# Kernel optimization log

Measured on AMD Instinct MI355X. Metric: run time of the kernel, lower is better.

Reference implementation:

```python
import jax, jax.numpy as jnp
import numpy as np

N = 1048576        # number of raw proposals
NC = 2             # num classes (source hardcodes self.nc = 2)
CONF_THRES = 0.25  # score_thres
IOU_THRES = 0.45
MAX_WH = 4096.0    # class offset for class-aware NMS (agnostic=False)
MAX_NMS = 30000    # cap on boxes entering NMS
MAX_DET = 300      # cap on detections returned


def setup_inputs() -> dict:
    key = jax.random.key(0)
    k1, k2, k3, k4 = jax.random.split(key, 4)
    xy = jax.random.uniform(k1, (1, N, 2), dtype=jnp.float32) * 640.0          # box centers (pixels)
    wh = jax.random.uniform(k2, (1, N, 2), dtype=jnp.float32) * 98.0 + 2.0     # widths/heights in [2, 100]
    obj = jax.random.uniform(k3, (1, N, 1), dtype=jnp.float32)                 # objectness
    cls = jax.random.uniform(k4, (1, N, NC), dtype=jnp.float32)                # class scores
    prediction = jnp.concatenate([xy, wh, obj, cls], axis=-1)                  # [1, N, 4+1+nc]
    return {"prediction": prediction}


def reference(prediction):
    # Single image (source only ever fills/returns output[0]).
    pred = prediction[0]                        # [N, 7]
    obj = pred[:, 4]                            # objectness
    cls = pred[:, 5:5 + NC] * obj[:, None]      # conf = obj * cls  (nc > 1 branch)
    conf = jnp.max(cls, axis=-1)                # best-class confidence
    j = jnp.argmax(cls, axis=-1)                # best-class index

    # xywh -> xyxy
    xy, wh = pred[:, :2], pred[:, 2:4]
    box = jnp.concatenate([xy - wh * 0.5, xy + wh * 0.5], axis=-1)  # [N, 4]

    # candidate mask: obj > thres (xc) AND best-class conf > thres
    valid = (obj > CONF_THRES) & (conf > CONF_THRES)
    scores = jnp.where(valid, conf, -1.0)

    # n > max_nms: keep top MAX_NMS by confidence (argsort descending truncation)
    top_s, top_i = jax.lax.top_k(scores, MAX_NMS)       # [MAX_NMS]
    box_t = box[top_i]                                   # [MAX_NMS, 4]
    conf_t = conf[top_i]
    j_t = j[top_i]

    # class-aware NMS: offset boxes per class so classes never suppress each other
    boxes_off = box_t + (j_t.astype(box_t.dtype) * MAX_WH)[:, None]
    area = (boxes_off[:, 2] - boxes_off[:, 0]) * (boxes_off[:, 3] - boxes_off[:, 1])

    # Greedy NMS: iteratively select max-score box, suppress IoU > thres.
    # Selecting the argmax each step is equivalent to sorted greedy NMS, and
    # MAX_DET steps yields exactly the first max_det kept indices.
    def step(s, _):
        idx = jnp.argmax(s)
        ok = s[idx] > 0.0                       # any real candidate left?
        b = boxes_off[idx]
        lt = jnp.maximum(b[:2], boxes_off[:, :2])
        rb = jnp.minimum(b[2:], boxes_off[:, 2:])
        inter = jnp.prod(jnp.clip(rb - lt, 0.0), axis=-1)
        iou = inter / (area[idx] + area - inter)
        s = jnp.where(ok & (iou > IOU_THRES), -1.0, s)  # suppress (incl. self, IoU=1)
        return s, (idx, ok)

    _, (sel, ok) = jax.lax.scan(step, top_s, None, length=MAX_DET)

    dets = jnp.concatenate(
        [box_t[sel], conf_t[sel, None], j_t[sel, None].astype(box_t.dtype)], axis=-1
    )                                           # [MAX_DET, 6] = [xyxy, conf, cls]
    dets = dets * ok[:, None].astype(dets.dtype)  # zero out padding rows
    return dets, ok
```

## Files before the change

kernel.cpp:

```cpp
#include <hip/hip_runtime.h>
#include <stdint.h>

#pragma clang fp contract(off)

#define N_ELEM   1048576
#define MAX_NMS  30000
#define MAX_DET  300
#define IOU_T    0.45f
#define CONF_T   0.25f
#define SOA_N    30720
#define KMIN     0xBE800000u
#define EQCAP    2048
#define RPW      16

typedef uint32_t u32;
typedef unsigned long long u64;

#define C_CB   0
#define C_KP   1
#define C_A    2
#define C_NUM  3
#define C_EQC  4

__device__ inline u32 monokey(float s){
  u32 b = __float_as_uint(s);
  return b ^ ((b & 0x80000000u) ? 0xFFFFFFFFu : 0x80000000u);
}
__device__ inline int binOf(u32 k){
  u32 d = (k - KMIN) >> 8;
  return d > 65535u ? 65535 : (int)d;
}
__device__ inline u64 shfl64(u64 v, int src){
  int lo = __shfl((int)(u32)(v & 0xFFFFFFFFull), src);
  int hi = __shfl((int)(u32)(v >> 32), src);
  return ((u64)(u32)hi << 32) | (u32)lo;
}

__global__ void kkeys(const float4* __restrict__ pred4, u32* __restrict__ keys,
                      u32* __restrict__ hist){
  __shared__ float lds[1792];
  int t = threadIdx.x;
  const float4* src = pred4 + (size_t)blockIdx.x * 448;
  float4* l4 = (float4*)lds;
  #pragma unroll
  for (int k = 0; k < 2; k++){
    int idx = k*256 + t;
    if (idx < 448) l4[idx] = src[idx];
  }
  __syncthreads();
  float obj = lds[t*7 + 4], c0 = lds[t*7 + 5], c1 = lds[t*7 + 6];
  float p0 = c0*obj, p1 = c1*obj;
  float conf = fmaxf(p0, p1);
  bool valid = (obj > CONF_T) && (conf > CONF_T);
  float score = valid ? conf : -1.0f;
  u32 mk = monokey(score);
  keys[blockIdx.x*256 + t] = mk;
  if (mk > KMIN) atomicAdd(&hist[binOf(mk)], 1u);
}

__global__ void kchunks(const u32* __restrict__ hist, u32* __restrict__ chunkSum){
  int gw = (blockIdx.x*blockDim.x + threadIdx.x) >> 6;
  int lane = threadIdx.x & 63;
  if (gw >= 1024) return;
  u32 v = hist[gw*64 + lane];
  #pragma unroll
  for (int off = 32; off > 0; off >>= 1) v += __shfl_down(v, off);
  if (lane == 0) chunkSum[gw] = v;
}

__global__ void kpick(const u32* __restrict__ chunkSum, const u32* __restrict__ hist,
                      u32* __restrict__ chunkAbove, u32* __restrict__ ctrl){
  __shared__ u32 s[1024];
  __shared__ int selC;
  __shared__ u32 selAbove;
  __shared__ u32 chunk[64];
  int t = threadIdx.x;
  u32 own = chunkSum[t];
  s[t] = own; __syncthreads();
  for (int off = 1; off < 1024; off <<= 1){
    u32 v = s[t];
    u32 add = (t + off < 1024) ? s[t + off] : 0u;
    __syncthreads();
    s[t] = v + add;
    __syncthreads();
  }
  u32 above = s[t] - own;
  chunkAbove[t] = above;
  u32 grand = s[0];
  const u32 K = MAX_NMS;
  if (grand >= K){
    if (above < K && K <= above + own){ selC = t; selAbove = above; }
  }
  __syncthreads();
  if (grand >= K && t < 64) chunk[t] = hist[selC*64 + t];
  __syncthreads();
  if (t == 0){
    if (grand < K){
      ctrl[C_CB] = 0xFFFFFFFFu; ctrl[C_KP] = 0; ctrl[C_A] = grand; ctrl[C_NUM] = grand;
    } else {
      u32 cum = selAbove;
      for (int b = 63; b >= 0; b--){
        u32 c = chunk[b];
        if (cum + c >= K){
          ctrl[C_CB] = (u32)(selC*64 + b);
          ctrl[C_KP] = K - cum;
          ctrl[C_A]  = cum;
          ctrl[C_NUM] = K;
          break;
        }
        cum += c;
      }
    }
  }
}

__global__ void kbinbase(const u32* __restrict__ hist, const u32* __restrict__ chunkAbove,
                         u32* __restrict__ binBase){
  int gw = (blockIdx.x*blockDim.x + threadIdx.x) >> 6;
  int lane = threadIdx.x & 63;
  if (gw >= 1024) return;
  u32 v = hist[gw*64 + lane];
  u32 suf = v;
  #pragma unroll
  for (int off = 1; off < 64; off <<= 1){
    u32 o = __shfl_down(suf, off);
    suf += (lane + off < 64) ? o : 0u;
  }
  binBase[gw*64 + lane] = chunkAbove[gw] + suf - v;
}

__global__ void kscatter(const uint4* __restrict__ keys4, const u32* __restrict__ binBase,
                         u32* __restrict__ binCursor, u32* __restrict__ ctrl,
                         u32* __restrict__ binnedKey, u32* __restrict__ binnedIdx,
                         u32* __restrict__ eqKey, u32* __restrict__ eqIdx){
  int t = blockIdx.x*blockDim.x + threadIdx.x;
  if (t >= N_ELEM/4) return;
  int cb = (int)ctrl[C_CB];
  uint4 kv = keys4[t];
  u32 kk[4] = {kv.x, kv.y, kv.z, kv.w};
  #pragma unroll
  for (int r = 0; r < 4; r++){
    u32 k = kk[r];
    if (k <= KMIN) continue;
    int b = binOf(k);
    u32 i = (u32)(t*4 + r);
    if (b > cb){
      u32 pos = binBase[b] + atomicAdd(&binCursor[b], 1u);
      if (pos < MAX_NMS){ binnedKey[pos] = k; binnedIdx[pos] = i; }
    } else if (b == cb){
      u32 e = atomicAdd(&ctrl[C_EQC], 1u);
      if (e < EQCAP){ eqKey[e] = k; eqIdx[e] = i; }
    }
  }
}

__global__ void keq(u32* __restrict__ ctrl, const u32* __restrict__ eqKey,
                    const u32* __restrict__ eqIdx, u32* __restrict__ binnedKey,
                    u32* __restrict__ binnedIdx, u32* __restrict__ binHist){
  u32 Kp = ctrl[C_KP];
  if (Kp == 0) return;
  u32 cb = ctrl[C_CB], A = ctrl[C_A];
  u32 n = ctrl[C_EQC]; if (n > EQCAP) n = EQCAP;
  int lane = threadIdx.x;
  for (u32 e = (u32)lane; e < n; e += 64){
    u32 k = eqKey[e], i = eqIdx[e];
    u32 r = 0;
    for (u32 m = 0; m < n; m++){
      u32 km = eqKey[m], im = eqIdx[m];
      r += (km > k) || (km == k && im < i);
    }
    if (r < Kp){ binnedKey[A + r] = k; binnedIdx[A + r] = i; }
  }
  if (lane == 0) binHist[cb] = Kp;
}

__global__ void krank(const float* __restrict__ pred, const u32* __restrict__ binnedKey,
                      const u32* __restrict__ binnedIdx, const u32* __restrict__ binBase,
                      const u32* __restrict__ binHist, const u32* __restrict__ ctrl,
                      float* __restrict__ soa){
  int p = blockIdx.x*blockDim.x + threadIdx.x;
  int numCand = (int)ctrl[C_NUM];
  if (p >= numCand) return;
  u32 k = binnedKey[p]; u32 i = binnedIdx[p];
  if (i >= N_ELEM) i = 0;
  int b = binOf(k);
  u32 st = binBase[b], cnt = binHist[b];
  u32 r = st;
  for (u32 q = st; q < st + cnt; q++){
    u32 kq = binnedKey[q], iq = binnedIdx[q];
    if (kq > k || (kq == k && iq < i)) r++;
  }
  if (r >= (u32)numCand) return;
  const float* row = pred + (size_t)i*7;
  float x = row[0], y = row[1], w = row[2], hh = row[3];
  float obj = row[4], c0 = row[5], c1 = row[6];
  float p0 = c0*obj, p1 = c1*obj;
  float conf = fmaxf(p0, p1);
  float jf = (p0 >= p1) ? 0.0f : 1.0f;
  float bx1 = x - w*0.5f, by1 = y - hh*0.5f;
  float bx2 = x + w*0.5f, by2 = y + hh*0.5f;
  float off = jf * 4096.0f;
  float ox1 = bx1 + off, oy1 = by1 + off, ox2 = bx2 + off, oy2 = by2 + off;
  float area = (ox2 - ox1) * (oy2 - oy1);
  soa[r + 0*SOA_N] = ox1;  soa[r + 1*SOA_N] = oy1;
  soa[r + 2*SOA_N] = ox2;  soa[r + 3*SOA_N] = oy2;
  soa[r + 4*SOA_N] = area; soa[r + 5*SOA_N] = conf;
  soa[r + 6*SOA_N] = jf;
  soa[r + 7*SOA_N] = bx1;  soa[r + 8*SOA_N] = by1;
  soa[r + 9*SOA_N] = bx2;  soa[r +10*SOA_N] = by2;
}

__global__ void kmask(const float* __restrict__ soa, u64* __restrict__ mask,
                      int W, int WBsh, int nUnits){
  int lane = threadIdx.x & 63;
  int gw = (blockIdx.x*blockDim.x + threadIdx.x) >> 6;
  int nwaves = (gridDim.x*blockDim.x) >> 6;
  int WB = 1 << WBsh;
  for (int u = gw; u < nUnits; u += nwaves){
    int rowg = u >> WBsh;
    int w = u & (WB - 1);
    if (((w + 1) << 6) <= rowg*RPW) continue;
    int j = (w << 6) + lane;
    float cx1 = soa[j], cy1 = soa[j + SOA_N], cx2 = soa[j + 2*SOA_N],
          cy2 = soa[j + 3*SOA_N], ca = soa[j + 4*SOA_N];
    #pragma unroll
    for (int rr = 0; rr < RPW; rr++){
      int i = rowg*RPW + rr;
      if (w < (i >> 6)) continue;
      float rx1 = soa[i], ry1 = soa[i + SOA_N], rx2 = soa[i + 2*SOA_N],
            ry2 = soa[i + 3*SOA_N], ra = soa[i + 4*SOA_N];
      float ltx = fmaxf(rx1, cx1), lty = fmaxf(ry1, cy1);
      float rbx = fminf(rx2, cx2), rby = fminf(ry2, cy2);
      float iw = fmaxf(rbx - ltx, 0.0f), ih = fmaxf(rby - lty, 0.0f);
      float inter = iw * ih;
      float iou = inter / ((ra + ca) - inter);
      u64 m = __ballot(iou > IOU_T);
      if (lane == 0) mask[(size_t)i*WB + w] = m;
    }
  }
}

__global__ void __launch_bounds__(64) kwalk(const float* __restrict__ soa,
                                            const u64* __restrict__ mask,
                                            const u32* __restrict__ ctrl,
                                            float* __restrict__ out, int out_size,
                                            int W){
  __shared__ float kx1[320], ky1[320], kx2[320], ky2[320], ka[320];
  __shared__ u64 dlds[64];
  int lane = threadIdx.x;
  for (int o = lane; o < out_size; o += 64) out[o] = 0.0f;
  int numCand = (int)ctrl[C_NUM];
  int WB = W >> 6;
  int lim = numCand < W ? numCand : W;
  int nb = (lim + 63) >> 6;
  u64 rem0 = 0, rem1 = 0;
  int nsel = 0;

  u64 diag = 0;
  if (nb > 0 && lane < lim) diag = mask[(size_t)lane*WB + 0];

  for (int bi = 0; bi < nb && nsel < MAX_DET; bi++){
    u64 remw = (bi < 64) ? shfl64(rem0, bi) : shfl64(rem1, bi - 64);
    u64 w = ~remw;
    int rb = lim - (bi << 6);
    if (rb < 64) w &= ((1ull << rb) - 1ull);
    dlds[lane] = diag;
    __syncthreads();

    u64 diagn = 0;
    int inext = (bi + 1)*64 + lane;
    if (bi + 1 < nb && inext < lim) diagn = mask[(size_t)inext*WB + (bi + 1)];

    u64 sel = 0;
    int room = MAX_DET - nsel;
    while (w){
      int b = (int)__builtin_ctzll(w);
      sel |= (1ull << b);
      if (--room == 0) break;
      u64 rw = dlds[b];
      w &= ~rw;
      w &= ~(1ull << b);
    }
    int cnt = __popcll(sel);

    u64 s = sel;
    long long ids[8];
    #pragma unroll
    for (int q = 0; q < 8; q++){
      if (s){ ids[q] = (long long)((bi << 6) + __builtin_ctzll(s)); s &= s - 1; }
      else ids[q] = -1;
    }
    u64 a0[8], a1[8];
    #pragma unroll
    for (int q = 0; q < 8; q++){
      a0[q] = 0; a1[q] = 0;
      if (ids[q] >= 0){
        const u64* rp = mask + (size_t)ids[q]*WB;
        if (lane < WB)      a0[q] = rp[lane];
        if (64 + lane < WB) a1[q] = rp[64 + lane];
      }
    }

    if (lane < cnt){
      u64 t = sel;
      for (int q = 0; q < lane; q++) t &= t - 1;
      int b = (int)__builtin_ctzll(t);
      int i = (bi << 6) + b;
      int r = nsel + lane;
      kx1[r] = soa[i];            ky1[r] = soa[i + SOA_N];
      kx2[r] = soa[i + 2*SOA_N];  ky2[r] = soa[i + 3*SOA_N];
      ka[r]  = soa[i + 4*SOA_N];
      float* dr = out + r*6;
      dr[0] = soa[i + 7*SOA_N];  dr[1] = soa[i + 8*SOA_N];
      dr[2] = soa[i + 9*SOA_N];  dr[3] = soa[i + 10*SOA_N];
      dr[4] = soa[i + 5*SOA_N];  dr[5] = soa[i + 6*SOA_N];
      out[MAX_DET*6 + r] = 1.0f;
    }
    nsel += cnt;

    #pragma unroll
    for (int q = 0; q < 8; q++){ rem0 |= a0[q]; rem1 |= a1[q]; }

    while (s){
      long long ids2[8];
      #pragma unroll
      for (int q = 0; q < 8; q++){
        if (s){ ids2[q] = (long long)((bi << 6) + __builtin_ctzll(s)); s &= s - 1; }
        else ids2[q] = -1;
      }
      u64 b0[8], b1[8];
      #pragma unroll
      for (int q = 0; q < 8; q++){
        b0[q] = 0; b1[q] = 0;
        if (ids2[q] >= 0){
          const u64* rp = mask + (size_t)ids2[q]*WB;
          if (lane < WB)      b0[q] = rp[lane];
          if (64 + lane < WB) b1[q] = rp[64 + lane];
        }
      }
      #pragma unroll
      for (int q = 0; q < 8; q++){ rem0 |= b0[q]; rem1 |= b1[q]; }
    }
    diag = diagn;
    __syncthreads();
  }

  if (nsel < MAX_DET && numCand > W){
    for (int base = W; base < numCand && nsel < MAX_DET; base += 64){
      int li = base + lane;
      bool has = li < numCand;
      float cox1=0.f,coy1=0.f,cox2=0.f,coy2=0.f,car=1.f,csc=-1.f,ccl=0.f;
      float cbx1=0.f,cby1=0.f,cbx2=0.f,cby2=0.f;
      if (has){
        cox1 = soa[li]; coy1 = soa[li + SOA_N]; cox2 = soa[li + 2*SOA_N];
        coy2 = soa[li + 3*SOA_N]; car = soa[li + 4*SOA_N];
        csc = soa[li + 5*SOA_N]; ccl = soa[li + 6*SOA_N];
        cbx1 = soa[li + 7*SOA_N]; cby1 = soa[li + 8*SOA_N];
        cbx2 = soa[li + 9*SOA_N]; cby2 = soa[li + 10*SOA_N];
      }
      int m = min(64, numCand - base);
      for (int t2 = 0; t2 < m && nsel < MAX_DET; t2++){
        float qx1 = __shfl(cox1, t2), qy1 = __shfl(coy1, t2);
        float qx2 = __shfl(cox2, t2), qy2 = __shfl(coy2, t2);
        float qa  = __shfl(car,  t2);
        bool supp = false;
        #pragma unroll
        for (int q = 0; q < 5; q++){
          int slot = lane + (q << 6);
          if (slot < nsel){
            float ltx = fmaxf(qx1, kx1[slot]), lty = fmaxf(qy1, ky1[slot]);
            float rbx = fminf(qx2, kx2[slot]), rby = fminf(qy2, ky2[slot]);
            float iw = fmaxf(rbx - ltx, 0.0f), ih = fmaxf(rby - lty, 0.0f);
            float inter = iw * ih;
            float iou = inter / ((qa + ka[slot]) - inter);
            supp = supp || (iou > IOU_T);
          }
        }
        if (__any(supp)) continue;
        float bx1 = __shfl(cbx1, t2), by1 = __shfl(cby1, t2);
        float bx2 = __shfl(cbx2, t2), by2 = __shfl(cby2, t2);
        float sc  = __shfl(csc,  t2), cl  = __shfl(ccl,  t2);
        if (lane == 0){
          kx1[nsel] = qx1; ky1[nsel] = qy1; kx2[nsel] = qx2; ky2[nsel] = qy2; ka[nsel] = qa;
          float* dr = out + nsel*6;
          dr[0] = bx1; dr[1] = by1; dr[2] = bx2; dr[3] = by2; dr[4] = sc; dr[5] = cl;
          out[MAX_DET*6 + nsel] = 1.0f;
        }
        nsel++;
      }
    }
  }
}

extern "C" void kernel_launch(void* const* d_in, const int* in_sizes, int n_in,
                              void* d_out, int out_size, void* d_ws, size_t ws_size,
                              hipStream_t stream){
  const float* pred = (const float*)d_in[0];
  float* out = (float*)d_out;
  char* w = (char*)d_ws;

  u32*  keys       = (u32*)(w + 0x000000);
  u32*  hist       = (u32*)(w + 0x400000);
  u32*  binCursor  = (u32*)(w + 0x440000);
  u32*  ctrl       = (u32*)(w + 0x480000);
  u32*  chunkSum   = (u32*)(w + 0x484000);
  u32*  chunkAbove = (u32*)(w + 0x488000);
  u32*  binBase    = (u32*)(w + 0x4C0000);
  u32*  eqKey      = (u32*)(w + 0x500000);
  u32*  eqIdx      = (u32*)(w + 0x502000);
  u32*  binnedKey  = (u32*)(w + 0x510000);
  u32*  binnedIdx  = (u32*)(w + 0x530000);
  float* soa       = (float*)(w + 0x550000);
  u64*  mask       = (u64*)(w + 0x6A0000);

  int W, WBsh;
  if      (ws_size >= 0xEA0000){ W = 8192; WBsh = 7; }
  else if (ws_size >= 0x8A0000){ W = 4096; WBsh = 6; }
  else                         { W = 2048; WBsh = 5; }

  hipMemsetAsync(hist, 0, 0x80100, stream);

  kkeys   <<<4096, 256, 0, stream>>>((const float4*)pred, keys, hist);
  kchunks <<<256, 256, 0, stream>>>(hist, chunkSum);
  kpick   <<<1, 1024, 0, stream>>>(chunkSum, hist, chunkAbove, ctrl);
  kbinbase<<<256, 256, 0, stream>>>(hist, chunkAbove, binBase);
  kscatter<<<1024, 256, 0, stream>>>((const uint4*)keys, binBase, binCursor, ctrl,
                                     binnedKey, binnedIdx, eqKey, eqIdx);
  keq     <<<1, 64, 0, stream>>>(ctrl, eqKey, eqIdx, binnedKey, binnedIdx, hist);
  krank   <<<(MAX_NMS + 255)/256, 256, 0, stream>>>(pred, binnedKey, binnedIdx, binBase,
                                                    hist, ctrl, soa);
  int nUnits = (W/RPW) << WBsh;
  kmask   <<<2048, 256, 0, stream>>>(soa, mask, W, WBsh, nUnits);
  kwalk   <<<1, 64, 0, stream>>>(soa, mask, ctrl, out, out_size, W);
}
```

Before: 285.9 us.

## Fuse chunk-sum, pick and bin-base kernels; fold tie-bin ranking into krank

Merges the three small histogram-scan kernels (kchunks, kpick, kbinbase) into one 1024-thread kselect kernel, so chunk sums and prefix offsets stay in shared memory. The single-wave keq kernel that ranked boundary-bin ties is removed; krank now ranks those ties in parallel across threads and writes their SoA rows directly. This cuts three kernel launches and their global round trips, and turns a serial 64-lane loop into a wide parallel pass. The cost is that the whole 64K-bin histogram is now read and scanned by a single workgroup, which may be slower than spreading it over 256 blocks.

Result: slower. 325.3 us (+13.8%).

```diff
diff --git a/kernel.cpp b/kernel.cpp
--- a/kernel.cpp
+++ b/kernel.cpp
@@ -58,24 +58,23 @@
   if (mk > KMIN) atomicAdd(&hist[binOf(mk)], 1u);
 }
 
-__global__ void kchunks(const u32* __restrict__ hist, u32* __restrict__ chunkSum){
-  int gw = (blockIdx.x*blockDim.x + threadIdx.x) >> 6;
-  int lane = threadIdx.x & 63;
-  if (gw >= 1024) return;
-  u32 v = hist[gw*64 + lane];
-  #pragma unroll
-  for (int off = 32; off > 0; off >>= 1) v += __shfl_down(v, off);
-  if (lane == 0) chunkSum[gw] = v;
-}
-
-__global__ void kpick(const u32* __restrict__ chunkSum, const u32* __restrict__ hist,
-                      u32* __restrict__ chunkAbove, u32* __restrict__ ctrl){
+__global__ void __launch_bounds__(1024) kselect(const u32* __restrict__ hist,
+                                                u32* __restrict__ binBase,
+                                                u32* __restrict__ ctrl){
+  __shared__ u32 csum[1024];
   __shared__ u32 s[1024];
   __shared__ int selC;
-  __shared__ u32 selAbove;
   __shared__ u32 chunk[64];
-  int t = threadIdx.x;
-  u32 own = chunkSum[t];
+  int t = threadIdx.x, lane = t & 63, wv = t >> 6;
+  for (int j = 0; j < 64; j++){
+    int c = wv*64 + j;
+    u32 v = hist[c*64 + lane];
+    #pragma unroll
+    for (int off = 32; off > 0; off >>= 1) v += __shfl_down(v, off);
+    if (lane == 0) csum[c] = v;
+  }
+  __syncthreads();
+  u32 own = csum[t];
   s[t] = own; __syncthreads();
   for (int off = 1; off < 1024; off <<= 1){
     u32 v = s[t];
@@ -85,12 +84,10 @@
     __syncthreads();
   }
   u32 above = s[t] - own;
-  chunkAbove[t] = above;
   u32 grand = s[0];
+  csum[t] = above;
   const u32 K = MAX_NMS;
-  if (grand >= K){
-    if (above < K && K <= above + own){ selC = t; selAbove = above; }
-  }
+  if (grand >= K && above < K && K <= above + own){ selC = t; }
   __syncthreads();
   if (grand >= K && t < 64) chunk[t] = hist[selC*64 + t];
   __syncthreads();
@@ -98,7 +95,7 @@
     if (grand < K){
       ctrl[C_CB] = 0xFFFFFFFFu; ctrl[C_KP] = 0; ctrl[C_A] = grand; ctrl[C_NUM] = grand;
     } else {
-      u32 cum = selAbove;
+      u32 cum = csum[selC];
       for (int b = 63; b >= 0; b--){
         u32 c = chunk[b];
         if (cum + c >= K){
@@ -112,21 +109,17 @@
       }
     }
   }
-}
-
-__global__ void kbinbase(const u32* __restrict__ hist, const u32* __restrict__ chunkAbove,
-                         u32* __restrict__ binBase){
-  int gw = (blockIdx.x*blockDim.x + threadIdx.x) >> 6;
-  int lane = threadIdx.x & 63;
-  if (gw >= 1024) return;
-  u32 v = hist[gw*64 + lane];
-  u32 suf = v;
-  #pragma unroll
-  for (int off = 1; off < 64; off <<= 1){
-    u32 o = __shfl_down(suf, off);
-    suf += (lane + off < 64) ? o : 0u;
-  }
-  binBase[gw*64 + lane] = chunkAbove[gw] + suf - v;
+  for (int j = 0; j < 64; j++){
+    int c = wv*64 + j;
+    u32 v = hist[c*64 + lane];
+    u32 suf = v;
+    #pragma unroll
+    for (int off = 1; off < 64; off <<= 1){
+      u32 o = __shfl_down(suf, off);
+      suf += (lane + off < 64) ? o : 0u;
+    }
+    binBase[c*64 + lane] = csum[c] + suf - v;
+  }
 }
 
 __global__ void kscatter(const uint4* __restrict__ keys4, const u32* __restrict__ binBase,
@@ -154,43 +147,8 @@
   }
 }
 
-__global__ void keq(u32* __restrict__ ctrl, const u32* __restrict__ eqKey,
-                    const u32* __restrict__ eqIdx, u32* __restrict__ binnedKey,
-                    u32* __restrict__ binnedIdx, u32* __restrict__ binHist){
-  u32 Kp = ctrl[C_KP];
-  if (Kp == 0) return;
-  u32 cb = ctrl[C_CB], A = ctrl[C_A];
-  u32 n = ctrl[C_EQC]; if (n > EQCAP) n = EQCAP;
-  int lane = threadIdx.x;
-  for (u32 e = (u32)lane; e < n; e += 64){
-    u32 k = eqKey[e], i = eqIdx[e];
-    u32 r = 0;
-    for (u32 m = 0; m < n; m++){
-      u32 km = eqKey[m], im = eqIdx[m];
-      r += (km > k) || (km == k && im < i);
-    }
-    if (r < Kp){ binnedKey[A + r] = k; binnedIdx[A + r] = i; }
-  }
-  if (lane == 0) binHist[cb] = Kp;
-}
-
-__global__ void krank(const float* __restrict__ pred, const u32* __restrict__ binnedKey,
-                      const u32* __restrict__ binnedIdx, const u32* __restrict__ binBase,
-                      const u32* __restrict__ binHist, const u32* __restrict__ ctrl,
-                      float* __restrict__ soa){
-  int p = blockIdx.x*blockDim.x + threadIdx.x;
-  int numCand = (int)ctrl[C_NUM];
-  if (p >= numCand) return;
-  u32 k = binnedKey[p]; u32 i = binnedIdx[p];
-  if (i >= N_ELEM) i = 0;
-  int b = binOf(k);
-  u32 st = binBase[b], cnt = binHist[b];
-  u32 r = st;
-  for (u32 q = st; q < st + cnt; q++){
-    u32 kq = binnedKey[q], iq = binnedIdx[q];
-    if (kq > k || (kq == k && iq < i)) r++;
-  }
-  if (r >= (u32)numCand) return;
+__device__ inline void writeSoA(const float* __restrict__ pred, float* __restrict__ soa,
+                                u32 r, u32 i){
   const float* row = pred + (size_t)i*7;
   float x = row[0], y = row[1], w = row[2], hh = row[3];
   float obj = row[4], c0 = row[5], c1 = row[6];
@@ -208,6 +166,39 @@
   soa[r + 6*SOA_N] = jf;
   soa[r + 7*SOA_N] = bx1;  soa[r + 8*SOA_N] = by1;
   soa[r + 9*SOA_N] = bx2;  soa[r +10*SOA_N] = by2;
+}
+
+__global__ void krank(const float* __restrict__ pred, const u32* __restrict__ binnedKey,
+                      const u32* __restrict__ binnedIdx, const u32* __restrict__ binBase,
+                      const u32* __restrict__ binHist, const u32* __restrict__ ctrl,
+                      const u32* __restrict__ eqKey, const u32* __restrict__ eqIdx,
+                      float* __restrict__ soa){
+  int p = blockIdx.x*blockDim.x + threadIdx.x;
+  u32 A = ctrl[C_A], Kp = ctrl[C_KP];
+  if (Kp > 0){
+    u32 n = ctrl[C_EQC]; if (n > EQCAP) n = EQCAP;
+    if (p < (int)n){
+      u32 k = eqKey[p], i = eqIdx[p];
+      u32 r = 0;
+      for (u32 m = 0; m < n; m++){
+        u32 km = eqKey[m], im = eqIdx[m];
+        r += (km > k) || (km == k && im < i);
+      }
+      if (r < Kp) writeSoA(pred, soa, A + r, i);
+    }
+  }
+  if (p < (int)A){
+    u32 k = binnedKey[p]; u32 i = binnedIdx[p];
+    if (i >= N_ELEM) i = 0;
+    int b = binOf(k);
+    u32 st = binBase[b], cnt = binHist[b];
+    u32 r = st;
+    for (u32 q = st; q < st + cnt; q++){
+      u32 kq = binnedKey[q], iq = binnedIdx[q];
+      if (kq > k || (kq == k && iq < i)) r++;
+    }
+    if (r < A) writeSoA(pred, soa, r, i);
+  }
 }
 
 __global__ void kmask(const float* __restrict__ soa, u64* __restrict__ mask,
@@ -403,8 +394,6 @@
   u32*  hist       = (u32*)(w + 0x400000);
   u32*  binCursor  = (u32*)(w + 0x440000);
   u32*  ctrl       = (u32*)(w + 0x480000);
-  u32*  chunkSum   = (u32*)(w + 0x484000);
-  u32*  chunkAbove = (u32*)(w + 0x488000);
   u32*  binBase    = (u32*)(w + 0x4C0000);
   u32*  eqKey      = (u32*)(w + 0x500000);
   u32*  eqIdx      = (u32*)(w + 0x502000);
@@ -421,14 +410,11 @@
   hipMemsetAsync(hist, 0, 0x80100, stream);
 
   kkeys   <<<4096, 256, 0, stream>>>((const float4*)pred, keys, hist);
-  kchunks <<<256, 256, 0, stream>>>(hist, chunkSum);
-  kpick   <<<1, 1024, 0, stream>>>(chunkSum, hist, chunkAbove, ctrl);
-  kbinbase<<<256, 256, 0, stream>>>(hist, chunkAbove, binBase);
+  kselect <<<1, 1024, 0, stream>>>(hist, binBase, ctrl);
   kscatter<<<1024, 256, 0, stream>>>((const uint4*)keys, binBase, binCursor, ctrl,
                                      binnedKey, binnedIdx, eqKey, eqIdx);
-  keq     <<<1, 64, 0, stream>>>(ctrl, eqKey, eqIdx, binnedKey, binnedIdx, hist);
-  krank   <<<(MAX_NMS + 255)/256, 256, 0, stream>>>(pred, binnedKey, binnedIdx, binBase,
-                                                    hist, ctrl, soa);
+  krank   <<<(MAX_NMS + 255)/256 + 1, 256, 0, stream>>>(pred, binnedKey, binnedIdx, binBase,
+                                                        hist, ctrl, eqKey, eqIdx, soa);
   int nUnits = (W/RPW) << WBsh;
   kmask   <<<2048, 256, 0, stream>>>(soa, mask, W, WBsh, nUnits);
   kwalk   <<<1, 64, 0, stream>>>(soa, mask, ctrl, out, out_size, W);
```
